# Optimization experiments

Hardware: AMD Instinct MI355X
Metric: run time of the kernel (lower is better)

The kernel has to match this reference:

```python
import jax, jax.numpy as jnp
import numpy as np

N = 512
C = 64
B = 1048576


def setup_inputs() -> dict:
    key = jax.random.key(0)
    k1, k2, k3, k4 = jax.random.split(key, 4)
    coords = jax.random.uniform(k1, (B, 3), dtype=jnp.float32, minval=-0.5, maxval=0.5)
    x_line = jax.random.normal(k2, (N, C), dtype=jnp.float32)
    y_line = jax.random.normal(k3, (N, C), dtype=jnp.float32)
    z_line = jax.random.normal(k4, (N, C), dtype=jnp.float32)
    grid = jnp.linspace(-0.5, 0.5, N, dtype=jnp.float32)
    return {"coords": coords, "x_line": x_line, "y_line": y_line, "z_line": z_line, "grid": grid}


def _interp_1d(line_feat, coord, grid):
    # line_feat: [N, C], coord: [B] in [-0.5, 0.5]
    n = line_feat.shape[0]
    pos = (coord - grid[0]) / (grid[1] - grid[0])          # [B] fractional index
    idx0 = jnp.clip(jnp.floor(pos).astype(jnp.int32), 0, n - 2)
    w1 = (pos - idx0.astype(pos.dtype))[:, None]            # [B, 1]
    f0 = line_feat[idx0]                                    # [B, C] gather
    f1 = line_feat[idx0 + 1]                                # [B, C] gather
    return f0 * (1.0 - w1) + f1 * w1


def reference(coords, x_line, y_line, z_line, grid):
    # mode='sum' (default): fx + fy + fz -> [B, C]
    fx = _interp_1d(x_line, coords[:, 0], grid)
    fy = _interp_1d(y_line, coords[:, 1], grid)
    fz = _interp_1d(z_line, coords[:, 2], grid)
    return fx + fy + fz
```

## Files before the change

### kernel.cpp

```cpp
#include <hip/hip_runtime.h>


typedef float f4 __attribute__((ext_vector_type(4)));

constexpr int kN       = 512;
constexpr int kC4      = 16;
constexpr int kGroups  = 4;
constexpr int kPr      = 64;
constexpr int kRowF    = 20;
constexpr int kThreads = 1024;
constexpr int kSlab    = 256;

__global__ __launch_bounds__(kThreads, 4) void triline_v3(
    const float* __restrict__ coords,
    const f4* __restrict__ xl,
    const f4* __restrict__ yl,
    const f4* __restrict__ zl,
    const float* __restrict__ grid,
    f4* __restrict__ out,
    int B)
{
    __shared__ float sm[3 * kN * kRowF];

    const int bid = blockIdx.x;
    const int g   = bid / kPr;
    const int pr  = bid % kPr;

    for (int i = threadIdx.x; i < kN * 4; i += kThreads) {
        const int r   = i >> 2;
        const int kk  = i & 3;
        const int dst = r * kRowF + kk * 4;
        const int src = r * kC4 + g * 4 + kk;
        *(f4*)&sm[dst]                  = xl[src];
        *(f4*)&sm[kN * kRowF + dst]     = yl[src];
        *(f4*)&sm[2 * kN * kRowF + dst] = zl[src];
    }
    __syncthreads();

    const float g0     = grid[0];
    const float inv_dg = 1.0f / (grid[1] - g0);

    const int p    = threadIdx.x >> 2;
    const int kw   = (threadIdx.x & 3) * 4;
    const int kout = g * 4 + (threadIdx.x & 3);

    const int per  = B / kPr;
    const int b0   = pr * per;
    const int bend = b0 + per;

    const float* sx = sm;
    const float* sy = sm + kN * kRowF;
    const float* sz = sm + 2 * kN * kRowF;

    int bA = b0 + p;
    float cxA = coords[3*bA+0], cyA = coords[3*bA+1], czA = coords[3*bA+2];

    float pxA = (cxA - g0) * inv_dg;
    float pyA = (cyA - g0) * inv_dg;
    float pzA = (czA - g0) * inv_dg;
    int ixA = min(max((int)floorf(pxA), 0), kN - 2);
    int iyA = min(max((int)floorf(pyA), 0), kN - 2);
    int izA = min(max((int)floorf(pzA), 0), kN - 2);
    float wxA = pxA - (float)ixA;
    float wyA = pyA - (float)iyA;
    float wzA = pzA - (float)izA;
    f4 Ax0 = *(const f4*)&sx[ixA * kRowF + kw];
    f4 Ax1 = *(const f4*)&sx[ixA * kRowF + kRowF + kw];
    f4 Ay0 = *(const f4*)&sy[iyA * kRowF + kw];
    f4 Ay1 = *(const f4*)&sy[iyA * kRowF + kRowF + kw];
    f4 Az0 = *(const f4*)&sz[izA * kRowF + kw];
    f4 Az1 = *(const f4*)&sz[izA * kRowF + kRowF + kw];

    int bB = bA + kSlab;
    int bBs = min(bB, bend - 1);
    float cxB = coords[3*bBs+0], cyB = coords[3*bBs+1], czB = coords[3*bBs+2];

    const int nIter = per / kSlab;
    for (int t = 0; t < nIter; t += 2) {
        float pxB = (cxB - g0) * inv_dg;
        float pyB = (cyB - g0) * inv_dg;
        float pzB = (czB - g0) * inv_dg;
        int ixB = min(max((int)floorf(pxB), 0), kN - 2);
        int iyB = min(max((int)floorf(pyB), 0), kN - 2);
        int izB = min(max((int)floorf(pzB), 0), kN - 2);
        float wxB = pxB - (float)ixB;
        float wyB = pyB - (float)iyB;
        float wzB = pzB - (float)izB;
        f4 Bx0 = *(const f4*)&sx[ixB * kRowF + kw];
        f4 Bx1 = *(const f4*)&sx[ixB * kRowF + kRowF + kw];
        f4 By0 = *(const f4*)&sy[iyB * kRowF + kw];
        f4 By1 = *(const f4*)&sy[iyB * kRowF + kRowF + kw];
        f4 Bz0 = *(const f4*)&sz[izB * kRowF + kw];
        f4 Bz1 = *(const f4*)&sz[izB * kRowF + kRowF + kw];

        const int bN1  = bA + 2 * kSlab;
        const int bN1s = min(bN1, bend - 1);
        float cxN = coords[3*bN1s+0], cyN = coords[3*bN1s+1], czN = coords[3*bN1s+2];

        f4 rA = Ax0 + (Ax1 - Ax0) * wxA;
        rA    = rA + Ay0 + (Ay1 - Ay0) * wyA;
        rA    = rA + Az0 + (Az1 - Az0) * wzA;
        out[bA * kC4 + kout] = rA;

        bA = bN1;
        float pxA2 = (cxN - g0) * inv_dg;
        float pyA2 = (cyN - g0) * inv_dg;
        float pzA2 = (czN - g0) * inv_dg;
        int ixA2 = min(max((int)floorf(pxA2), 0), kN - 2);
        int iyA2 = min(max((int)floorf(pyA2), 0), kN - 2);
        int izA2 = min(max((int)floorf(pzA2), 0), kN - 2);
        wxA = pxA2 - (float)ixA2;
        wyA = pyA2 - (float)iyA2;
        wzA = pzA2 - (float)izA2;
        Ax0 = *(const f4*)&sx[ixA2 * kRowF + kw];
        Ax1 = *(const f4*)&sx[ixA2 * kRowF + kRowF + kw];
        Ay0 = *(const f4*)&sy[iyA2 * kRowF + kw];
        Ay1 = *(const f4*)&sy[iyA2 * kRowF + kRowF + kw];
        Az0 = *(const f4*)&sz[izA2 * kRowF + kw];
        Az1 = *(const f4*)&sz[izA2 * kRowF + kRowF + kw];

        const int bN2  = bB + 2 * kSlab;
        const int bN2s = min(bN2, bend - 1);
        cxB = coords[3*bN2s+0];
        cyB = coords[3*bN2s+1];
        czB = coords[3*bN2s+2];

        f4 rB = Bx0 + (Bx1 - Bx0) * wxB;
        rB    = rB + By0 + (By1 - By0) * wyB;
        rB    = rB + Bz0 + (Bz1 - Bz0) * wzB;
        out[bB * kC4 + kout] = rB;
        bB = bN2;
    }
}

extern "C" void kernel_launch(void* const* d_in, const int* in_sizes, int n_in,
                              void* d_out, int out_size, void* d_ws, size_t ws_size,
                              hipStream_t stream) {
    const float* coords = (const float*)d_in[0];
    const f4*    xl     = (const f4*)d_in[1];
    const f4*    yl     = (const f4*)d_in[2];
    const f4*    zl     = (const f4*)d_in[3];
    const float* grid   = (const float*)d_in[4];
    f4*          out    = (f4*)d_out;

    int B = in_sizes[0] / 3;

    triline_v3<<<kGroups * kPr, kThreads, 0, stream>>>(
        coords, xl, yl, zl, grid, out, B);
}
```

Before: 326.3 us.

## Store line tables in fp16 LDS and compute 8 channels per thread

The line feature tables are converted to fp16 in shared memory, so each block can hold 32 channels instead of 16. Each thread now produces 8 channels with packed half arithmetic. The grid is 2 channel groups times 128 point ranges instead of 4 times 64, so coords are read half as often per output. Output writes become nontemporal stores. The cost is reduced precision, since features, weights and accumulation are all fp16, which may exceed the tolerance.

After: 321.8 us. No clear change (-1.4%).

```diff
diff --git a/kernel.cpp b/kernel.cpp
--- a/kernel.cpp
+++ b/kernel.cpp
@@ -1,17 +1,17 @@
 #include <hip/hip_runtime.h>
 
 
-typedef float f4 __attribute__((ext_vector_type(4)));
+typedef float    f4 __attribute__((ext_vector_type(4)));
+typedef _Float16 h8 __attribute__((ext_vector_type(8)));
 
 constexpr int kN       = 512;
 constexpr int kC4      = 16;
-constexpr int kGroups  = 4;
-constexpr int kPr      = 64;
-constexpr int kRowF    = 20;
+constexpr int kPr      = 128;
+constexpr int kRowH    = 40;
 constexpr int kThreads = 1024;
 constexpr int kSlab    = 256;
 
-__global__ __launch_bounds__(kThreads, 4) void triline_v3(
+__global__ __launch_bounds__(kThreads, 4) void triline_v4(
     const float* __restrict__ coords,
     const f4* __restrict__ xl,
     const f4* __restrict__ yl,
@@ -20,37 +20,48 @@
     f4* __restrict__ out,
     int B)
 {
-    __shared__ float sm[3 * kN * kRowF];
+    __shared__ _Float16 sm[3 * kN * kRowH];
 
     const int bid = blockIdx.x;
-    const int g   = bid / kPr;
-    const int pr  = bid % kPr;
+    const int g   = bid >> 7;
+    const int pr  = bid & 127;
 
-    for (int i = threadIdx.x; i < kN * 4; i += kThreads) {
-        const int r   = i >> 2;
-        const int kk  = i & 3;
-        const int dst = r * kRowF + kk * 4;
-        const int src = r * kC4 + g * 4 + kk;
-        *(f4*)&sm[dst]                  = xl[src];
-        *(f4*)&sm[kN * kRowF + dst]     = yl[src];
-        *(f4*)&sm[2 * kN * kRowF + dst] = zl[src];
+    for (int i = threadIdx.x; i < 3 * kN * 2; i += kThreads) {
+        const int tb  = i >> 10;
+        const int rem = i & 1023;
+        const int r   = rem >> 1;
+        const int h   = rem & 1;
+        const f4* src = (tb == 0) ? xl : (tb == 1) ? yl : zl;
+        const int sb  = r * kC4 + g * 8 + h * 4;
+        const f4 a0 = src[sb + 0], a1 = src[sb + 1];
+        const f4 a2 = src[sb + 2], a3 = src[sb + 3];
+        h8 lo, hi;
+        lo[0]=(_Float16)a0.x; lo[1]=(_Float16)a0.y; lo[2]=(_Float16)a0.z; lo[3]=(_Float16)a0.w;
+        lo[4]=(_Float16)a1.x; lo[5]=(_Float16)a1.y; lo[6]=(_Float16)a1.z; lo[7]=(_Float16)a1.w;
+        hi[0]=(_Float16)a2.x; hi[1]=(_Float16)a2.y; hi[2]=(_Float16)a2.z; hi[3]=(_Float16)a2.w;
+        hi[4]=(_Float16)a3.x; hi[5]=(_Float16)a3.y; hi[6]=(_Float16)a3.z; hi[7]=(_Float16)a3.w;
+        _Float16* dst = &sm[tb * kN * kRowH + r * kRowH + h * 16];
+        *(h8*)&dst[0] = lo;
+        *(h8*)&dst[8] = hi;
     }
     __syncthreads();
 
     const float g0     = grid[0];
     const float inv_dg = 1.0f / (grid[1] - g0);
 
-    const int p    = threadIdx.x >> 2;
-    const int kw   = (threadIdx.x & 3) * 4;
-    const int kout = g * 4 + (threadIdx.x & 3);
+    const int p  = threadIdx.x >> 2;
+    const int k  = threadIdx.x & 3;
+    const int kh = k * 8;
 
     const int per  = B / kPr;
     const int b0   = pr * per;
     const int bend = b0 + per;
 
-    const float* sx = sm;
-    const float* sy = sm + kN * kRowF;
-    const float* sz = sm + 2 * kN * kRowF;
+    const _Float16* sx = sm;
+    const _Float16* sy = sm + kN * kRowH;
+    const _Float16* sz = sm + 2 * kN * kRowH;
+
+    const int coutA = g * 8 + 2 * k;
 
     int bA = b0 + p;
     float cxA = coords[3*bA+0], cyA = coords[3*bA+1], czA = coords[3*bA+2];
@@ -61,17 +72,17 @@
     int ixA = min(max((int)floorf(pxA), 0), kN - 2);
     int iyA = min(max((int)floorf(pyA), 0), kN - 2);
     int izA = min(max((int)floorf(pzA), 0), kN - 2);
-    float wxA = pxA - (float)ixA;
-    float wyA = pyA - (float)iyA;
-    float wzA = pzA - (float)izA;
-    f4 Ax0 = *(const f4*)&sx[ixA * kRowF + kw];
-    f4 Ax1 = *(const f4*)&sx[ixA * kRowF + kRowF + kw];
-    f4 Ay0 = *(const f4*)&sy[iyA * kRowF + kw];
-    f4 Ay1 = *(const f4*)&sy[iyA * kRowF + kRowF + kw];
-    f4 Az0 = *(const f4*)&sz[izA * kRowF + kw];
-    f4 Az1 = *(const f4*)&sz[izA * kRowF + kRowF + kw];
+    _Float16 wxA = (_Float16)(pxA - (float)ixA);
+    _Float16 wyA = (_Float16)(pyA - (float)iyA);
+    _Float16 wzA = (_Float16)(pzA - (float)izA);
+    h8 Ax0 = *(const h8*)&sx[ixA * kRowH + kh];
+    h8 Ax1 = *(const h8*)&sx[ixA * kRowH + kRowH + kh];
+    h8 Ay0 = *(const h8*)&sy[iyA * kRowH + kh];
+    h8 Ay1 = *(const h8*)&sy[iyA * kRowH + kRowH + kh];
+    h8 Az0 = *(const h8*)&sz[izA * kRowH + kh];
+    h8 Az1 = *(const h8*)&sz[izA * kRowH + kRowH + kh];
 
-    int bB = bA + kSlab;
+    int bB  = bA + kSlab;
     int bBs = min(bB, bend - 1);
     float cxB = coords[3*bBs+0], cyB = coords[3*bBs+1], czB = coords[3*bBs+2];
 
@@ -83,24 +94,29 @@
         int ixB = min(max((int)floorf(pxB), 0), kN - 2);
         int iyB = min(max((int)floorf(pyB), 0), kN - 2);
         int izB = min(max((int)floorf(pzB), 0), kN - 2);
-        float wxB = pxB - (float)ixB;
-        float wyB = pyB - (float)iyB;
-        float wzB = pzB - (float)izB;
-        f4 Bx0 = *(const f4*)&sx[ixB * kRowF + kw];
-        f4 Bx1 = *(const f4*)&sx[ixB * kRowF + kRowF + kw];
-        f4 By0 = *(const f4*)&sy[iyB * kRowF + kw];
-        f4 By1 = *(const f4*)&sy[iyB * kRowF + kRowF + kw];
-        f4 Bz0 = *(const f4*)&sz[izB * kRowF + kw];
-        f4 Bz1 = *(const f4*)&sz[izB * kRowF + kRowF + kw];
+        _Float16 wxB = (_Float16)(pxB - (float)ixB);
+        _Float16 wyB = (_Float16)(pyB - (float)iyB);
+        _Float16 wzB = (_Float16)(pzB - (float)izB);
+        h8 Bx0 = *(const h8*)&sx[ixB * kRowH + kh];
+        h8 Bx1 = *(const h8*)&sx[ixB * kRowH + kRowH + kh];
+        h8 By0 = *(const h8*)&sy[iyB * kRowH + kh];
+        h8 By1 = *(const h8*)&sy[iyB * kRowH + kRowH + kh];
+        h8 Bz0 = *(const h8*)&sz[izB * kRowH + kh];
+        h8 Bz1 = *(const h8*)&sz[izB * kRowH + kRowH + kh];
 
         const int bN1  = bA + 2 * kSlab;
         const int bN1s = min(bN1, bend - 1);
         float cxN = coords[3*bN1s+0], cyN = coords[3*bN1s+1], czN = coords[3*bN1s+2];
 
-        f4 rA = Ax0 + (Ax1 - Ax0) * wxA;
-        rA    = rA + Ay0 + (Ay1 - Ay0) * wyA;
-        rA    = rA + Az0 + (Az1 - Az0) * wzA;
-        out[bA * kC4 + kout] = rA;
+        {
+            h8 acc = Ax0 + (Ax1 - Ax0) * wxA;
+            acc    = acc + Ay0 + (Ay1 - Ay0) * wyA;
+            acc    = acc + Az0 + (Az1 - Az0) * wzA;
+            f4 o0 = { (float)acc[0], (float)acc[1], (float)acc[2], (float)acc[3] };
+            f4 o1 = { (float)acc[4], (float)acc[5], (float)acc[6], (float)acc[7] };
+            __builtin_nontemporal_store(o0, &out[bA * kC4 + coutA]);
+            __builtin_nontemporal_store(o1, &out[bA * kC4 + coutA + 1]);
+        }
 
         bA = bN1;
         float pxA2 = (cxN - g0) * inv_dg;
@@ -109,15 +125,15 @@
         int ixA2 = min(max((int)floorf(pxA2), 0), kN - 2);
         int iyA2 = min(max((int)floorf(pyA2), 0), kN - 2);
         int izA2 = min(max((int)floorf(pzA2), 0), kN - 2);
-        wxA = pxA2 - (float)ixA2;
-        wyA = pyA2 - (float)iyA2;
-        wzA = pzA2 - (float)izA2;
-        Ax0 = *(const f4*)&sx[ixA2 * kRowF + kw];
-        Ax1 = *(const f4*)&sx[ixA2 * kRowF + kRowF + kw];
-        Ay0 = *(const f4*)&sy[iyA2 * kRowF + kw];
-        Ay1 = *(const f4*)&sy[iyA2 * kRowF + kRowF + kw];
-        Az0 = *(const f4*)&sz[izA2 * kRowF + kw];
-        Az1 = *(const f4*)&sz[izA2 * kRowF + kRowF + kw];
+        wxA = (_Float16)(pxA2 - (float)ixA2);
+        wyA = (_Float16)(pyA2 - (float)iyA2);
+        wzA = (_Float16)(pzA2 - (float)izA2);
+        Ax0 = *(const h8*)&sx[ixA2 * kRowH + kh];
+        Ax1 = *(const h8*)&sx[ixA2 * kRowH + kRowH + kh];
+        Ay0 = *(const h8*)&sy[iyA2 * kRowH + kh];
+        Ay1 = *(const h8*)&sy[iyA2 * kRowH + kRowH + kh];
+        Az0 = *(const h8*)&sz[izA2 * kRowH + kh];
+        Az1 = *(const h8*)&sz[izA2 * kRowH + kRowH + kh];
 
         const int bN2  = bB + 2 * kSlab;
         const int bN2s = min(bN2, bend - 1);
@@ -125,10 +141,15 @@
         cyB = coords[3*bN2s+1];
         czB = coords[3*bN2s+2];
 
-        f4 rB = Bx0 + (Bx1 - Bx0) * wxB;
-        rB    = rB + By0 + (By1 - By0) * wyB;
-        rB    = rB + Bz0 + (Bz1 - Bz0) * wzB;
-        out[bB * kC4 + kout] = rB;
+        {
+            h8 acc = Bx0 + (Bx1 - Bx0) * wxB;
+            acc    = acc + By0 + (By1 - By0) * wyB;
+            acc    = acc + Bz0 + (Bz1 - Bz0) * wzB;
+            f4 o0 = { (float)acc[0], (float)acc[1], (float)acc[2], (float)acc[3] };
+            f4 o1 = { (float)acc[4], (float)acc[5], (float)acc[6], (float)acc[7] };
+            __builtin_nontemporal_store(o0, &out[bB * kC4 + coutA]);
+            __builtin_nontemporal_store(o1, &out[bB * kC4 + coutA + 1]);
+        }
         bB = bN2;
     }
 }
@@ -145,6 +166,6 @@
 
     int B = in_sizes[0] / 3;
 
-    triline_v3<<<kGroups * kPr, kThreads, 0, stream>>>(
+    triline_v4<<<2 * kPr, kThreads, 0, stream>>>(
         coords, xl, yl, zl, grid, out, B);
 }
```
